# Optimization experiments

Measured on AMD Instinct MI355X. Metric: run time of the kernel, lower is better.

Reference implementation:

```python
import jax, jax.numpy as jnp
import numpy as np

HIDDEN = 4096
N_HEADS = 32
N_KV_HEADS = 8
HEAD_DIM = HIDDEN // N_HEADS  # 128
N_REP = N_HEADS // N_KV_HEADS  # 4
ROPE_THETA = 10000.0
B, S = 2, 2048


def setup_inputs() -> dict:
    key = jax.random.key(0)
    ks = jax.random.split(key, 9)
    sc = 1.0 / np.sqrt(HIDDEN)
    query = jax.random.normal(ks[0], (B, S, HIDDEN), jnp.float32)
    key_t = jax.random.normal(ks[1], (B, S, HIDDEN), jnp.float32)
    value = jax.random.normal(ks[2], (B, S, HIDDEN), jnp.float32)
    position_ids = jnp.sort(jax.random.randint(ks[3], (B, S), 0, S), axis=-1)
    Wq = jax.random.normal(ks[4], (HIDDEN, N_HEADS * HEAD_DIM), jnp.float32) * sc
    Wk = jax.random.normal(ks[5], (HIDDEN, N_KV_HEADS * HEAD_DIM), jnp.float32) * sc
    Wv = jax.random.normal(ks[6], (HIDDEN, N_KV_HEADS * HEAD_DIM), jnp.float32) * sc
    Wo = jax.random.normal(ks[7], (N_HEADS * HEAD_DIM, HIDDEN), jnp.float32) * sc
    return {"query": query, "key": key_t, "value": value,
            "position_ids": position_ids,
            "Wq": Wq, "Wk": Wk, "Wv": Wv, "Wo": Wo}


def _rotate_half(x):
    x1, x2 = jnp.split(x, 2, axis=-1)
    return jnp.concatenate((-x2, x1), axis=-1)


def _rope_cos_sin(position_ids):
    # inv_freq: [head_dim/2]
    inv_freq = 1.0 / (ROPE_THETA ** (jnp.arange(0, HEAD_DIM, 2, dtype=jnp.float32) / HEAD_DIM))
    # freqs: [B, S, head_dim/2] via per-position lookup (equiv. to cache gather cos_cached[position_ids])
    freqs = position_ids[..., None].astype(jnp.float32) * inv_freq
    emb = jnp.concatenate((freqs, freqs), axis=-1)          # [B, S, head_dim]
    return jnp.cos(emb)[:, None, :, :], jnp.sin(emb)[:, None, :, :]  # [B,1,S,hd]


def reference(query, key, value, position_ids, Wq, Wk, Wv, Wo):
    nb, q_len, _ = query.shape
    # QKV projections (bias-free linear)
    q = jnp.einsum('bse,ef->bsf', query, Wq).reshape(nb, q_len, N_HEADS, HEAD_DIM).transpose(0, 2, 1, 3)
    k = jnp.einsum('bse,ef->bsf', key, Wk).reshape(nb, q_len, N_KV_HEADS, HEAD_DIM).transpose(0, 2, 1, 3)
    v = jnp.einsum('bse,ef->bsf', value, Wv).reshape(nb, q_len, N_KV_HEADS, HEAD_DIM).transpose(0, 2, 1, 3)
    # RoPE
    cos, sin = _rope_cos_sin(position_ids)
    q = q * cos + _rotate_half(q) * sin
    k = k * cos + _rotate_half(k) * sin
    # GQA repeat_kv: [B, kvH, S, d] -> [B, H, S, d]
    k = jnp.repeat(k, N_REP, axis=1)
    v = jnp.repeat(v, N_REP, axis=1)
    # scaled dot-product attention (flash-attn semantics, no padding mask)
    scale = 1.0 / jnp.sqrt(jnp.asarray(HEAD_DIM, q.dtype))
    scores = jnp.einsum('bhqd,bhkd->bhqk', q, k) * scale
    probs = jax.nn.softmax(scores, axis=-1)
    ctx = jnp.einsum('bhqk,bhkd->bhqd', probs, v)
    ctx = ctx.transpose(0, 2, 1, 3).reshape(nb, q_len, N_HEADS * HEAD_DIM)
    return jnp.einsum('bsf,fe->bse', ctx, Wo)
```

## Files before the change

kernel.cpp:

```cpp
#include <hip/hip_runtime.h>
#include <hip/hip_bf16.h>

typedef __attribute__((ext_vector_type(8))) short bf16x8;
typedef __attribute__((ext_vector_type(4))) float f32x4;
typedef __attribute__((ext_vector_type(16))) float f32x16;
typedef __attribute__((ext_vector_type(2))) unsigned uint2x;

#define AS1(p) ((const __attribute__((address_space(1))) void*)(p))
#define AS3(p) ((__attribute__((address_space(3))) void*)(p))

__device__ inline unsigned cvtpk_bf16(float lo, float hi) {
  unsigned r;
  asm("v_cvt_pk_bf16_f32 %0, %1, %2" : "=v"(r) : "v"(lo), "v"(hi));
  return r;
}

__device__ inline uint2x plswap(unsigned a, unsigned b) {
  return __builtin_amdgcn_permlane32_swap(a, b, false, false);
}


__global__ __launch_bounds__(256) void xconv_kv(const float* __restrict__ k_in,
                                                const float* __restrict__ v_in,
                                                __hip_bfloat16* __restrict__ kc,
                                                __hip_bfloat16* __restrict__ vc) {
  const float* in = blockIdx.y ? v_in : k_in;
  __hip_bfloat16* out = blockIdx.y ? vc : kc;
  size_t i = ((size_t)blockIdx.x * 256 + threadIdx.x) * 4;
  float4 v = *(const float4*)(in + i);
  union { __hip_bfloat16 h[4]; ushort4 u; } o;
  o.h[0] = __float2bfloat16(v.x);
  o.h[1] = __float2bfloat16(v.y);
  o.h[2] = __float2bfloat16(v.z);
  o.h[3] = __float2bfloat16(v.w);
  *(ushort4*)(out + i) = o.u;
}

__global__ __launch_bounds__(256) void xconv(const float* __restrict__ in,
                                             __hip_bfloat16* __restrict__ out) {
  size_t i = ((size_t)blockIdx.x * 256 + threadIdx.x) * 4;
  float4 v = *(const float4*)(in + i);
  union { __hip_bfloat16 h[4]; ushort4 u; } o;
  o.h[0] = __float2bfloat16(v.x);
  o.h[1] = __float2bfloat16(v.y);
  o.h[2] = __float2bfloat16(v.z);
  o.h[3] = __float2bfloat16(v.w);
  *(ushort4*)(out + i) = o.u;
}

__global__ __launch_bounds__(256) void wtransAll(const float* __restrict__ Wq,
                                                 const float* __restrict__ Wo,
                                                 const float* __restrict__ Wk,
                                                 const float* __restrict__ Wv,
                                                 __hip_bfloat16* __restrict__ WqT,
                                                 __hip_bfloat16* __restrict__ WoT,
                                                 __hip_bfloat16* __restrict__ WkT,
                                                 __hip_bfloat16* __restrict__ WvT) {
  const int z = blockIdx.z;
  const int N = (z < 2) ? 4096 : 1024;
  const int n0 = blockIdx.x << 5;
  if (n0 >= N) return;
  const float* W = (z == 0) ? Wq : (z == 1) ? Wo : (z == 2) ? Wk : Wv;
  __hip_bfloat16* WT = (z == 0) ? WqT : (z == 1) ? WoT : (z == 2) ? WkT : WvT;
  __shared__ float t[32][33];
  const int k0 = blockIdx.y << 5;
  const int tx = threadIdx.x, ty = threadIdx.y;
#pragma unroll
  for (int j = 0; j < 4; ++j)
    t[ty + j * 8][tx] = W[(size_t)(k0 + ty + j * 8) * N + n0 + tx];
  __syncthreads();
#pragma unroll
  for (int j = 0; j < 4; ++j)
    WT[(size_t)(n0 + ty + j * 8) * 4096 + k0 + tx] = __float2bfloat16(t[tx][ty + j * 8]);
}

__global__ __launch_bounds__(256) void rope2(__hip_bfloat16* __restrict__ Qp,
                                             __hip_bfloat16* __restrict__ Kp,
                                             const int* __restrict__ pos, float qs) {
  int bid = blockIdx.x;
  __hip_bfloat16* X;
  int hbits; float scale; int t;
  if (bid < 32768) { X = Qp; hbits = 5; scale = qs; t = bid * 256 + threadIdx.x; }
  else { X = Kp; hbits = 3; scale = 1.0f; t = (bid - 32768) * 256 + threadIdx.x; }
  const int j = t & 63;
  const int rest = t >> 6;
  const int h = rest & ((1 << hbits) - 1);
  const int row = rest >> hbits;
  const float p = (float)pos[row];
  const float fr = p * exp2f((float)j * -0.2076205059304601f);
  float sn, cs;
  __sincosf(fr, &sn, &cs);
  const size_t base = (((size_t)row << hbits) + h) * 128 + j;
  const float x0 = __bfloat162float(X[base]);
  const float x1 = __bfloat162float(X[base + 64]);
  X[base]      = __float2bfloat16((x0 * cs - x1 * sn) * scale);
  X[base + 64] = __float2bfloat16((x1 * cs + x0 * sn) * scale);
}

__global__ __launch_bounds__(256) void gemm_kv(const __hip_bfloat16* __restrict__ Ak,
                                               const __hip_bfloat16* __restrict__ Av,
                                               const __hip_bfloat16* __restrict__ BkT,
                                               const __hip_bfloat16* __restrict__ BvT,
                                               __hip_bfloat16* __restrict__ Kp,
                                               __hip_bfloat16* __restrict__ VT) {
  __shared__ __align__(16) __hip_bfloat16 sh[17408];
  __hip_bfloat16* As = sh;
  __hip_bfloat16* Bs = sh + 8192;
  const int zz = blockIdx.z;
  const __hip_bfloat16* A  = zz ? Av : Ak;
  const __hip_bfloat16* BT = zz ? BvT : BkT;
  const int K = 4096, N = 1024;
  const int tid = threadIdx.x;
  const int lane = tid & 63, w = tid >> 6;
  const int m0 = blockIdx.y * 128, n0 = blockIdx.x * 128;
  const int wr = (w >> 1) * 64, wc = (w & 1) * 64;
  const int l15 = lane & 15, lg = lane >> 4;

  f32x4 acc[4][4] = {};
  const int srow = lane >> 3;
  const int scol = (lane & 7) * 8;

  for (int k0 = 0; k0 < K; k0 += 64) {
    __syncthreads();
#pragma unroll
    for (int i = 0; i < 4; ++i) {
      const int chunk = i * 4 + w;
      const int row = chunk * 8 + srow;
      __builtin_amdgcn_global_load_lds(AS1(A + (size_t)(m0 + row) * K + k0 + scol),
                                       AS3(As + chunk * 512), 16, 0, 0);
      __builtin_amdgcn_global_load_lds(AS1(BT + (size_t)(n0 + row) * K + k0 + scol),
                                       AS3(Bs + chunk * 512), 16, 0, 0);
    }
    __syncthreads();
#pragma unroll
    for (int kk = 0; kk < 2; ++kk) {
      bf16x8 af[4], bfr[4];
#pragma unroll
      for (int r = 0; r < 4; ++r) {
        af[r]  = *(const bf16x8*)(As + (wr + r * 16 + l15) * 64 + kk * 32 + lg * 8);
        bfr[r] = *(const bf16x8*)(Bs + (wc + r * 16 + l15) * 64 + kk * 32 + lg * 8);
      }
#pragma unroll
      for (int r = 0; r < 4; ++r)
#pragma unroll
        for (int c = 0; c < 4; ++c)
          acc[r][c] = __builtin_amdgcn_mfma_f32_16x16x32_bf16(af[r], bfr[c], acc[r][c], 0, 0, 0);
    }
  }

  if (zz == 0) {
#pragma unroll
    for (int r = 0; r < 4; ++r)
#pragma unroll
      for (int c = 0; c < 4; ++c)
#pragma unroll
        for (int i = 0; i < 4; ++i)
          Kp[(size_t)(m0 + wr + r * 16 + lg * 4 + i) * N + n0 + wc + c * 16 + l15] =
              __float2bfloat16(acc[r][c][i]);
  } else {
    __syncthreads();
    __hip_bfloat16* T = sh;
#pragma unroll
    for (int r = 0; r < 4; ++r)
#pragma unroll
      for (int c = 0; c < 4; ++c) {
        const int col = wc + c * 16 + l15;
        const int row = wr + r * 16 + lg * 4;
        union { __hip_bfloat16 h[4]; unsigned long long u; } pkv;
#pragma unroll
        for (int i = 0; i < 4; ++i) pkv.h[i] = __float2bfloat16(acc[r][c][i]);
        *(unsigned long long*)(T + col * 136 + row) = pkv.u;
      }
    __syncthreads();
    const int b = m0 >> 11, s0g = m0 & 2047, g = n0 >> 7;
    __hip_bfloat16* Vh = VT + (size_t)(b * 8 + g) * 128 * 2048;
    const int chunk = tid & 15;
#pragma unroll
    for (int it = 0; it < 8; ++it) {
      const int d = it * 16 + (tid >> 4);
      bf16x8 vv = *(const bf16x8*)(T + d * 136 + chunk * 8);
      *(bf16x8*)(Vh + (size_t)d * 2048 + s0g + chunk * 8) = vv;
    }
  }
}


__device__ inline int tile_off(int row, int k) {
  return (((row >> 4) << 1) + (k >> 5)) * 512 + (row & 15) * 32 +
         ((k & 31) ^ ((row & 8) << 1));
}

__device__ inline void stageA(const __hip_bfloat16* __restrict__ src, int ld, int row0,
                              int kt, int h, __hip_bfloat16* ldsT, int w, int lane) {
#pragma unroll
  for (int li = 0; li < 2; ++li) {
    const int t = li * 8 + w;
    const int grp = ((t >> 3) << 1) + h;
    const int srl = (t & 7) >> 1, sk = t & 1;
    const int rowbase = grp * 64 + srl * 16;
    __hip_bfloat16* dst = ldsT + ((((rowbase >> 4) << 1) + sk) << 9);
    const int r = lane >> 2;
    const int ku = (lane & 3) ^ ((r & 8) >> 2);
    __builtin_amdgcn_global_load_lds(
        AS1(src + (size_t)(row0 + rowbase + r) * ld + kt + (sk << 5) + (ku << 3)),
        AS3(dst), 16, 0, 0);
  }
}

__device__ inline void stageB(const __hip_bfloat16* __restrict__ src, int ld, int col0,
                              int kt, int h, __hip_bfloat16* ldsT, int w, int lane) {
#pragma unroll
  for (int li = 0; li < 2; ++li) {
    const int t = li * 8 + w;
    const int q = t >> 2;
    const int srl = (t >> 1) & 1, sk = t & 1;
    const int colbase = q * 64 + h * 32 + srl * 16;
    __hip_bfloat16* dst = ldsT + ((((colbase >> 4) << 1) + sk) << 9);
    const int r = lane >> 2;
    const int ku = (lane & 3) ^ ((r & 8) >> 2);
    __builtin_amdgcn_global_load_lds(
        AS1(src + (size_t)(col0 + colbase + r) * ld + kt + (sk << 5) + (ku << 3)),
        AS3(dst), 16, 0, 0);
  }
}

template <int OUT_F32>
__global__ __launch_bounds__(512, 1) void gemm256(const __hip_bfloat16* __restrict__ A,
                                                  const __hip_bfloat16* __restrict__ BT,
                                                  void* __restrict__ Cout,
                                                  int M, int N, int K) {
  __shared__ __align__(16) __hip_bfloat16 lds[2][2][16384];
  const int tid = threadIdx.x;
  const int lane = tid & 63, w = tid >> 6;
  const int l15 = lane & 15, lg = lane >> 4;
  const int wm = w >> 2, wn = w & 3;
  const int nbx = N >> 8;
  const int nwg = (M >> 8) * nbx;
  const int bid = blockIdx.x;
  const int swz = (bid & 7) * (nwg >> 3) + (bid >> 3);
  const int m0 = (swz / nbx) << 8, n0 = (swz % nbx) << 8;

  f32x4 acc[8][4] = {};
  const int NT = K >> 6;

  stageA(A, K, m0, 0, 0, &lds[0][0][0], w, lane);
  stageB(BT, K, n0, 0, 0, &lds[0][1][0], w, lane);
  stageA(A, K, m0, 0, 1, &lds[0][0][0], w, lane);
  stageB(BT, K, n0, 0, 1, &lds[0][1][0], w, lane);
  stageA(A, K, m0, 64, 0, &lds[1][0][0], w, lane);
  stageB(BT, K, n0, 64, 0, &lds[1][1][0], w, lane);
  asm volatile("s_waitcnt vmcnt(4)" ::: "memory");
  __builtin_amdgcn_s_barrier();

  for (int j = 0; j < NT; ++j) {
    const int buf = j & 1;
    const __hip_bfloat16* Ab = &lds[buf][0][0];
    const __hip_bfloat16* Bb = &lds[buf][1][0];
    __hip_bfloat16* An = &lds[buf ^ 1][0][0];
    __hip_bfloat16* Bn = &lds[buf ^ 1][1][0];
    __hip_bfloat16* Ac = &lds[buf][0][0];
    __hip_bfloat16* Bc = &lds[buf][1][0];
    const int kt1 = (j + 1) << 6, kt2 = (j + 2) << 6;
    const bool s1 = (j + 1) < NT, s2 = (j + 2) < NT;

    auto phase = [&](int rq, int cq, int sid) {
      bf16x8 af[2][4], bfr[2][2];
#pragma unroll
      for (int kk = 0; kk < 2; ++kk) {
#pragma unroll
        for (int rf = 0; rf < 4; ++rf)
          af[kk][rf] = *(const bf16x8*)(Ab +
              tile_off(wm * 128 + (rq * 4 + rf) * 16 + l15, kk * 32 + lg * 8));
#pragma unroll
        for (int cf = 0; cf < 2; ++cf)
          bfr[kk][cf] = *(const bf16x8*)(Bb +
              tile_off(wn * 64 + (cq * 2 + cf) * 16 + l15, kk * 32 + lg * 8));
      }
      if (sid == 0)      { if (s1) stageA(A, K, m0, kt1, 1, An, w, lane); }
      else if (sid == 1) { if (s1) stageB(BT, K, n0, kt1, 1, Bn, w, lane); }
      else if (sid == 2) { if (s2) stageA(A, K, m0, kt2, 0, Ac, w, lane); }
      else {
        if (s2) stageB(BT, K, n0, kt2, 0, Bc, w, lane);
        if (s2) asm volatile("s_waitcnt vmcnt(4)" ::: "memory");
        else    asm volatile("s_waitcnt vmcnt(0)" ::: "memory");
      }
      __builtin_amdgcn_s_barrier();
      asm volatile("s_waitcnt lgkmcnt(0)" ::: "memory");
      __builtin_amdgcn_sched_barrier(0);
      __builtin_amdgcn_s_setprio(1);
#pragma unroll
      for (int kk = 0; kk < 2; ++kk)
#pragma unroll
        for (int rf = 0; rf < 4; ++rf)
#pragma unroll
          for (int cf = 0; cf < 2; ++cf)
            acc[rq * 4 + rf][cq * 2 + cf] = __builtin_amdgcn_mfma_f32_16x16x32_bf16(
                af[kk][rf], bfr[kk][cf], acc[rq * 4 + rf][cq * 2 + cf], 0, 0, 0);
      __builtin_amdgcn_s_setprio(0);
      __builtin_amdgcn_s_barrier();
    };
    phase(0, 0, 0);
    phase(0, 1, 1);
    phase(1, 0, 2);
    phase(1, 1, 3);
  }

#pragma unroll
  for (int rf = 0; rf < 8; ++rf)
#pragma unroll
    for (int cf = 0; cf < 4; ++cf)
#pragma unroll
      for (int i = 0; i < 4; ++i) {
        const size_t row = (size_t)(m0 + wm * 128 + rf * 16 + lg * 4 + i);
        const size_t col = (size_t)(n0 + wn * 64 + cf * 16 + l15);
        if (OUT_F32)
          ((float*)Cout)[row * N + col] = acc[rf][cf][i];
        else
          ((__hip_bfloat16*)Cout)[row * N + col] = __float2bfloat16(acc[rf][cf][i]);
      }
}

__global__ __launch_bounds__(512) void attn(const __hip_bfloat16* __restrict__ Q,
                                            const __hip_bfloat16* __restrict__ Kp,
                                            const __hip_bfloat16* __restrict__ VT,
                                            __hip_bfloat16* __restrict__ ctx) {
  const int tid = threadIdx.x;
  const int lane = tid & 63, w = tid >> 6;
  const int l31 = lane & 31, hi = lane >> 5;
  const int qt = blockIdx.x, h = blockIdx.y, b = blockIdx.z;
  const int kvh = h >> 2;
  const int q0 = qt * 256 + w * 32;

  const __hip_bfloat16* Qh = Q + (size_t)(b * 2048) * 4096 + h * 128;
  const __hip_bfloat16* Kh = Kp + (size_t)(b * 2048) * 1024 + kvh * 128;
  const __hip_bfloat16* Vh = VT + (size_t)(b * 8 + kvh) * 128 * 2048;

  __shared__ __hip_bfloat16 Ks[2][64 * 128];
  __shared__ __hip_bfloat16 Vs[2][128 * 64];

  auto stage = [&](int buf, int s0) {
#pragma unroll
    for (int j = 0; j < 2; ++j) {
      const int idx = w * 64 + lane + j * 512;
      const int rK = idx >> 4, uK = idx & 15;
      __builtin_amdgcn_global_load_lds(
          AS1(Kh + (size_t)(s0 + rK) * 1024 + ((uK ^ (rK & 7)) << 3)),
          AS3(&Ks[buf][(w * 64 + j * 512) * 8]), 16, 0, 0);
      const int rV = idx >> 3, uV = idx & 7;
      __builtin_amdgcn_global_load_lds(
          AS1(Vh + (size_t)rV * 2048 + s0 + ((uV ^ (rV & 7)) << 3)),
          AS3(&Vs[buf][(w * 64 + j * 512) * 8]), 16, 0, 0);
    }
  };

  bf16x8 qf[8];
#pragma unroll
  for (int kd = 0; kd < 8; ++kd)
    qf[kd] = *(const bf16x8*)(Qh + (size_t)(q0 + l31) * 4096 + kd * 16 + hi * 8);

  f32x16 o[4] = {};
  float m = -1e30f, lsum = 0.f;

  stage(0, 0);
  __syncthreads();

  auto tile = [&](int tt, int cur, bool pf) {
    if (pf) stage(cur ^ 1, (tt + 1) * 64);

    f32x16 p[2] = {};
    __builtin_amdgcn_s_setprio(1);
#pragma unroll
    for (int n = 0; n < 2; ++n)
#pragma unroll
      for (int kd = 0; kd < 8; ++kd) {
        const int row = n * 32 + l31;
        bf16x8 kf = *(const bf16x8*)(&Ks[cur][row * 128 + (((2 * kd + hi) ^ (row & 7)) << 3)]);
        p[n] = __builtin_amdgcn_mfma_f32_32x32x16_bf16(kf, qf[kd], p[n], 0, 0, 0);
      }
    __builtin_amdgcn_s_setprio(0);

    float t16[16], t8[8], t4[4];
#pragma unroll
    for (int e = 0; e < 16; ++e) t16[e] = fmaxf(p[0][e], p[1][e]);
#pragma unroll
    for (int e = 0; e < 8; ++e) t8[e] = fmaxf(t16[e], t16[e + 8]);
#pragma unroll
    for (int e = 0; e < 4; ++e) t4[e] = fmaxf(t8[e], t8[e + 4]);
    float pmax = fmaxf(fmaxf(t4[0], t4[1]), fmaxf(t4[2], t4[3]));
    {
      uint2x r = plswap(__float_as_uint(pmax), __float_as_uint(pmax));
      pmax = fmaxf(__uint_as_float(r[0]), __uint_as_float(r[1]));
    }
    if (!__all(pmax - m <= 8.0f)) {
      const float mnew = fmaxf(m, pmax);
      const float fac = exp2f(m - mnew);
      m = mnew;
      lsum *= fac;
#pragma unroll
      for (int dc = 0; dc < 4; ++dc)
#pragma unroll
        for (int e = 0; e < 16; ++e) o[dc][e] *= fac;
    }
#pragma unroll
    for (int n = 0; n < 2; ++n)
#pragma unroll
      for (int e = 0; e < 16; ++e) p[n][e] = exp2f(p[n][e] - m);
    float s16[16];
#pragma unroll
    for (int e = 0; e < 16; ++e) s16[e] = p[0][e] + p[1][e];
#pragma unroll
    for (int e = 0; e < 8; ++e) s16[e] = s16[e] + s16[e + 8];
#pragma unroll
    for (int e = 0; e < 4; ++e) s16[e] = s16[e] + s16[e + 4];
    float rs = (s16[0] + s16[1]) + (s16[2] + s16[3]);
    {
      uint2x r = plswap(__float_as_uint(rs), __float_as_uint(rs));
      rs = __uint_as_float(r[0]) + __uint_as_float(r[1]);
    }
    lsum += rs;

    __builtin_amdgcn_s_setprio(1);
#pragma unroll
    for (int n = 0; n < 2; ++n)
#pragma unroll
      for (int ks = 0; ks < 2; ++ks) {
        const int bse = ks * 8;
        unsigned a1 = cvtpk_bf16(p[n][bse + 0], p[n][bse + 1]);
        unsigned b1 = cvtpk_bf16(p[n][bse + 4], p[n][bse + 5]);
        unsigned a2 = cvtpk_bf16(p[n][bse + 2], p[n][bse + 3]);
        unsigned b2 = cvtpk_bf16(p[n][bse + 6], p[n][bse + 7]);
        uint2x s1 = plswap(a1, b1);
        uint2x s2 = plswap(a2, b2);
        union { unsigned u[4]; bf16x8 v; } pw = {{s1[0], s2[0], s1[1], s2[1]}};
        const int slot = n * 2 + ks;
#pragma unroll
        for (int dc = 0; dc < 4; ++dc) {
          const int row = dc * 32 + l31;
          bf16x8 vf = *(const bf16x8*)(&Vs[cur][row * 64 + (((2 * slot + hi) ^ (row & 7)) << 3)]);
          o[dc] = __builtin_amdgcn_mfma_f32_32x32x16_bf16(vf, pw.v, o[dc], 0, 0, 0);
        }
      }
    __builtin_amdgcn_s_setprio(0);
    __syncthreads();
  };

  for (int t2 = 0; t2 < 16; ++t2) {
    tile(2 * t2, 0, true);
    tile(2 * t2 + 1, 1, t2 < 15);
  }

  const float inv = 1.0f / lsum;
  const size_t rowbase = ((size_t)(b * 2048 + q0 + l31)) * 4096 + h * 128;
#pragma unroll
  for (int dc = 0; dc < 4; ++dc)
#pragma unroll
    for (int g = 0; g < 4; ++g) {
      union { unsigned short us[4]; ushort4 u4; } pk;
#pragma unroll
      for (int e = 0; e < 4; ++e) {
        __hip_bfloat16 hv = __float2bfloat16(o[dc][g * 4 + e] * inv);
        pk.us[e] = *(unsigned short*)&hv;
      }
      *(ushort4*)(ctx + rowbase + dc * 32 + g * 8 + hi * 4) = pk.u4;
    }
}


extern "C" void kernel_launch(void* const* d_in, const int* in_sizes, int n_in,
                              void* d_out, int out_size, void* d_ws, size_t ws_size,
                              hipStream_t stream) {
  const float* q_in = (const float*)d_in[0];
  const float* k_in = (const float*)d_in[1];
  const float* v_in = (const float*)d_in[2];
  const int* pos    = (const int*)d_in[3];
  const float* Wq   = (const float*)d_in[4];
  const float* Wk   = (const float*)d_in[5];
  const float* Wv   = (const float*)d_in[6];
  const float* Wo   = (const float*)d_in[7];

  char* ws = (char*)d_ws;
  __hip_bfloat16* xbuf = (__hip_bfloat16*)(ws);
  __hip_bfloat16* WqT  = (__hip_bfloat16*)(ws + 33554432);
  __hip_bfloat16* WkT  = (__hip_bfloat16*)(ws + 67108864);
  __hip_bfloat16* WvT  = (__hip_bfloat16*)(ws + 75497472);
  __hip_bfloat16* WoT  = (__hip_bfloat16*)(ws + 83886080);
  __hip_bfloat16* Qp   = (__hip_bfloat16*)(ws + 117440512);
  __hip_bfloat16* Kp   = (__hip_bfloat16*)(ws + 150994944);
  __hip_bfloat16* VTb  = (__hip_bfloat16*)(ws + 167772160);
  __hip_bfloat16* vconv = WqT;

  wtransAll<<<dim3(128, 128, 4), dim3(32, 8), 0, stream>>>(Wq, Wo, Wk, Wv,
                                                           WqT, WoT, WkT, WvT);
  xconv<<<16384, 256, 0, stream>>>(q_in, xbuf);
  gemm256<0><<<256, 512, 0, stream>>>(xbuf, WqT, Qp, 4096, 4096, 4096);
  xconv_kv<<<dim3(16384, 2), 256, 0, stream>>>(k_in, v_in, xbuf, vconv);
  gemm_kv<<<dim3(8, 32, 2), 256, 0, stream>>>(xbuf, vconv, WkT, WvT, Kp, VTb);
  rope2<<<40960, 256, 0, stream>>>(Qp, Kp, pos,
                                   0.08838834764831845f * 1.4426950408889634f);
  attn<<<dim3(8, 32, 2), 512, 0, stream>>>(Qp, Kp, VTb, xbuf);
  gemm256<1><<<256, 512, 0, stream>>>(xbuf, WoT, d_out, 4096, 4096, 4096);
}
```

Measured before the change: 670.4 us.

## Fuse Q RoPE into attention prologue and pack softmax arithmetic

Applies the Q rotary embedding and the softmax scale inside the attention kernel while it loads Q fragments, so the separate RoPE pass touches only K. This removes a full read-modify-write of the Q projection through memory. The softmax max reduction is restructured, and the rescale, subtract-max and row-sum steps use packed two-wide f32 instructions to cut VALU instruction count. The cost is redundant sincos work per attention block, since each Q row is rotated by 8 waves across head tiles. The K-tile prefetch is now issued before the Q prologue so it overlaps that work.

```diff
diff --git a/kernel.cpp b/kernel.cpp
--- a/kernel.cpp
+++ b/kernel.cpp
@@ -4,6 +4,7 @@
 typedef __attribute__((ext_vector_type(8))) short bf16x8;
 typedef __attribute__((ext_vector_type(4))) float f32x4;
 typedef __attribute__((ext_vector_type(16))) float f32x16;
+typedef __attribute__((ext_vector_type(2))) float f32x2;
 typedef __attribute__((ext_vector_type(2))) unsigned uint2x;
 
 #define AS1(p) ((const __attribute__((address_space(1))) void*)(p))
@@ -17,6 +18,17 @@
 
 __device__ inline uint2x plswap(unsigned a, unsigned b) {
   return __builtin_amdgcn_permlane32_swap(a, b, false, false);
+}
+
+__device__ inline f32x2 pkadd(f32x2 a, f32x2 b) {
+  f32x2 d;
+  asm("v_pk_add_f32 %0, %1, %2" : "=v"(d) : "v"(a), "v"(b));
+  return d;
+}
+__device__ inline f32x2 pkmul(f32x2 a, f32x2 b) {
+  f32x2 d;
+  asm("v_pk_mul_f32 %0, %1, %2" : "=v"(d) : "v"(a), "v"(b));
+  return d;
 }
 
 
@@ -74,14 +86,10 @@
     WT[(size_t)(n0 + ty + j * 8) * 4096 + k0 + tx] = __float2bfloat16(t[tx][ty + j * 8]);
 }
 
-__global__ __launch_bounds__(256) void rope2(__hip_bfloat16* __restrict__ Qp,
-                                             __hip_bfloat16* __restrict__ Kp,
-                                             const int* __restrict__ pos, float qs) {
-  int bid = blockIdx.x;
-  __hip_bfloat16* X;
-  int hbits; float scale; int t;
-  if (bid < 32768) { X = Qp; hbits = 5; scale = qs; t = bid * 256 + threadIdx.x; }
-  else { X = Kp; hbits = 3; scale = 1.0f; t = (bid - 32768) * 256 + threadIdx.x; }
+__global__ __launch_bounds__(256) void rope(__hip_bfloat16* __restrict__ X,
+                                            const int* __restrict__ pos,
+                                            int hbits, float scale) {
+  const int t = blockIdx.x * 256 + threadIdx.x;
   const int j = t & 63;
   const int rest = t >> 6;
   const int h = rest & ((1 << hbits) - 1);
@@ -323,7 +331,9 @@
 __global__ __launch_bounds__(512) void attn(const __hip_bfloat16* __restrict__ Q,
                                             const __hip_bfloat16* __restrict__ Kp,
                                             const __hip_bfloat16* __restrict__ VT,
-                                            __hip_bfloat16* __restrict__ ctx) {
+                                            const int* __restrict__ pos,
+                                            __hip_bfloat16* __restrict__ ctx,
+                                            float qs) {
   const int tid = threadIdx.x;
   const int lane = tid & 63, w = tid >> 6;
   const int l31 = lane & 31, hi = lane >> 5;
@@ -353,15 +363,37 @@
     }
   };
 
+  stage(0, 0);
+
+  const int qrow = q0 + l31;
+  const float pp = (float)pos[b * 2048 + qrow];
   bf16x8 qf[8];
-#pragma unroll
-  for (int kd = 0; kd < 8; ++kd)
-    qf[kd] = *(const bf16x8*)(Qh + (size_t)(q0 + l31) * 4096 + kd * 16 + hi * 8);
+  {
+#pragma unroll
+    for (int kd = 0; kd < 4; ++kd) {
+      bf16x8 rlo = *(const bf16x8*)(Qh + (size_t)qrow * 4096 + kd * 16 + hi * 8);
+      bf16x8 rhi = *(const bf16x8*)(Qh + (size_t)qrow * 4096 + (kd + 4) * 16 + hi * 8);
+      bf16x8 olo, ohi;
+#pragma unroll
+      for (int e = 0; e < 8; ++e) {
+        const int j = kd * 16 + hi * 8 + e;
+        const float fr = pp * exp2f((float)j * -0.2076205059304601f);
+        float sn, cs;
+        __sincosf(fr, &sn, &cs);
+        const float x0 = __uint_as_float(((unsigned)(unsigned short)rlo[e]) << 16);
+        const float x1 = __uint_as_float(((unsigned)(unsigned short)rhi[e]) << 16);
+        __hip_bfloat16 h0 = __float2bfloat16((x0 * cs - x1 * sn) * qs);
+        __hip_bfloat16 h1 = __float2bfloat16((x1 * cs + x0 * sn) * qs);
+        olo[e] = *(short*)&h0;
+        ohi[e] = *(short*)&h1;
+      }
+      qf[kd] = olo;
+      qf[kd + 4] = ohi;
+    }
+  }
 
   f32x16 o[4] = {};
   float m = -1e30f, lsum = 0.f;
-
-  stage(0, 0);
   __syncthreads();
 
   auto tile = [&](int tt, int cur, bool pf) {
@@ -379,14 +411,15 @@
       }
     __builtin_amdgcn_s_setprio(0);
 
-    float t16[16], t8[8], t4[4];
+    float t16[16];
 #pragma unroll
     for (int e = 0; e < 16; ++e) t16[e] = fmaxf(p[0][e], p[1][e]);
-#pragma unroll
-    for (int e = 0; e < 8; ++e) t8[e] = fmaxf(t16[e], t16[e + 8]);
-#pragma unroll
-    for (int e = 0; e < 4; ++e) t4[e] = fmaxf(t8[e], t8[e + 4]);
-    float pmax = fmaxf(fmaxf(t4[0], t4[1]), fmaxf(t4[2], t4[3]));
+    const float u0 = fmaxf(fmaxf(t16[0], t16[1]), t16[2]);
+    const float u1 = fmaxf(fmaxf(t16[3], t16[4]), t16[5]);
+    const float u2 = fmaxf(fmaxf(t16[6], t16[7]), t16[8]);
+    const float u3 = fmaxf(fmaxf(t16[9], t16[10]), t16[11]);
+    const float u4 = fmaxf(fmaxf(t16[12], t16[13]), t16[14]);
+    float pmax = fmaxf(fmaxf(fmaxf(u0, u1), u2), fmaxf(fmaxf(u3, u4), t16[15]));
     {
       uint2x r = plswap(__float_as_uint(pmax), __float_as_uint(pmax));
       pmax = fmaxf(__uint_as_float(r[0]), __uint_as_float(r[1]));
@@ -396,23 +429,39 @@
       const float fac = exp2f(m - mnew);
       m = mnew;
       lsum *= fac;
+      f32x2 f2; f2[0] = fac; f2[1] = fac;
 #pragma unroll
       for (int dc = 0; dc < 4; ++dc)
 #pragma unroll
-        for (int e = 0; e < 16; ++e) o[dc][e] *= fac;
-    }
+        for (int i = 0; i < 8; ++i) {
+          f32x2 a; a[0] = o[dc][2 * i]; a[1] = o[dc][2 * i + 1];
+          a = pkmul(a, f2);
+          o[dc][2 * i] = a[0]; o[dc][2 * i + 1] = a[1];
+        }
+    }
+    f32x2 mneg; mneg[0] = -m; mneg[1] = -m;
 #pragma unroll
     for (int n = 0; n < 2; ++n)
 #pragma unroll
-      for (int e = 0; e < 16; ++e) p[n][e] = exp2f(p[n][e] - m);
-    float s16[16];
-#pragma unroll
-    for (int e = 0; e < 16; ++e) s16[e] = p[0][e] + p[1][e];
-#pragma unroll
-    for (int e = 0; e < 8; ++e) s16[e] = s16[e] + s16[e + 8];
-#pragma unroll
-    for (int e = 0; e < 4; ++e) s16[e] = s16[e] + s16[e + 4];
-    float rs = (s16[0] + s16[1]) + (s16[2] + s16[3]);
+      for (int i = 0; i < 8; ++i) {
+        f32x2 a; a[0] = p[n][2 * i]; a[1] = p[n][2 * i + 1];
+        a = pkadd(a, mneg);
+        p[n][2 * i] = exp2f(a[0]);
+        p[n][2 * i + 1] = exp2f(a[1]);
+      }
+    f32x2 s[8];
+#pragma unroll
+    for (int i = 0; i < 8; ++i) {
+      f32x2 a; a[0] = p[0][2 * i]; a[1] = p[0][2 * i + 1];
+      f32x2 bb; bb[0] = p[1][2 * i]; bb[1] = p[1][2 * i + 1];
+      s[i] = pkadd(a, bb);
+    }
+#pragma unroll
+    for (int i = 0; i < 4; ++i) s[i] = pkadd(s[i], s[i + 4]);
+    s[0] = pkadd(s[0], s[2]);
+    s[1] = pkadd(s[1], s[3]);
+    s[0] = pkadd(s[0], s[1]);
+    float rs = s[0][0] + s[0][1];
     {
       uint2x r = plswap(__float_as_uint(rs), __float_as_uint(rs));
       rs = __uint_as_float(r[0]) + __uint_as_float(r[1]);
@@ -495,8 +544,8 @@
   gemm256<0><<<256, 512, 0, stream>>>(xbuf, WqT, Qp, 4096, 4096, 4096);
   xconv_kv<<<dim3(16384, 2), 256, 0, stream>>>(k_in, v_in, xbuf, vconv);
   gemm_kv<<<dim3(8, 32, 2), 256, 0, stream>>>(xbuf, vconv, WkT, WvT, Kp, VTb);
-  rope2<<<40960, 256, 0, stream>>>(Qp, Kp, pos,
-                                   0.08838834764831845f * 1.4426950408889634f);
-  attn<<<dim3(8, 32, 2), 512, 0, stream>>>(Qp, Kp, VTb, xbuf);
+  rope<<<8192, 256, 0, stream>>>(Kp, pos, 3, 1.0f);
+  attn<<<dim3(8, 32, 2), 512, 0, stream>>>(Qp, Kp, VTb, pos, xbuf,
+                                           0.08838834764831845f * 1.4426950408889634f);
   gemm256<1><<<256, 512, 0, stream>>>(xbuf, WoT, d_out, 4096, 4096, 4096);
 }
```

New measurement: 662.4 us. About the same (-1.2%).
